# Kernel tuning notes

Hardware: AMD Instinct MI355X
Metric: run time of the kernel (lower is better)

## Reference

```python
import jax, jax.numpy as jnp
import numpy as np

LATENT = 1024

def setup_inputs() -> dict:
    key = jax.random.key(0)
    ks = jax.random.split(key, 8)
    N, BD, H, W = 1024, 2048, 7, 7
    C = 64  # num classes (pos == orient, required by stack dim=2)
    feat = jax.random.normal(ks[0], (N, BD, H, W), dtype=jnp.float32)
    fc1_w = jax.random.normal(ks[1], (LATENT, BD), dtype=jnp.float32) * (2.0 / BD) ** 0.5
    fc1_b = jnp.zeros((LATENT,), dtype=jnp.float32)
    cls_pos_w = jax.random.normal(ks[2], (C, LATENT), dtype=jnp.float32) * (2.0 / LATENT) ** 0.5
    cls_pos_b = jnp.zeros((C,), dtype=jnp.float32)
    cls_orient_w = jax.random.normal(ks[3], (C, LATENT), dtype=jnp.float32) * (2.0 / LATENT) ** 0.5
    cls_orient_b = jnp.zeros((C,), dtype=jnp.float32)
    reg_pos_w = jax.random.normal(ks[4], (C, 3, LATENT), dtype=jnp.float32) * (2.0 / LATENT) ** 0.5
    reg_pos_b = jnp.zeros((C, 3), dtype=jnp.float32)
    reg_orient_w = jax.random.normal(ks[5], (C, 4, LATENT), dtype=jnp.float32) * (2.0 / LATENT) ** 0.5
    reg_orient_b = jnp.zeros((C, 4), dtype=jnp.float32)
    return {"feat": feat, "fc1_w": fc1_w, "fc1_b": fc1_b,
            "cls_pos_w": cls_pos_w, "cls_pos_b": cls_pos_b,
            "cls_orient_w": cls_orient_w, "cls_orient_b": cls_orient_b,
            "reg_pos_w": reg_pos_w, "reg_pos_b": reg_pos_b,
            "reg_orient_w": reg_orient_w, "reg_orient_b": reg_orient_b}

def _to_label(pred):
    # relu(sum(cumprod(pred > 0.5, dim=1)) - 1) -> int64 ordinal label
    run = jnp.cumprod((pred > 0.5).astype(jnp.int32), axis=1)
    return jnp.maximum(run.sum(axis=1) - 1, 0).astype(jnp.int32)

def reference(feat, fc1_w, fc1_b, cls_pos_w, cls_pos_b, cls_orient_w, cls_orient_b,
              reg_pos_w, reg_pos_b, reg_orient_w, reg_orient_b):
    # AdaptiveAvgPool2d(1) + flatten -> [N, backbone_dim]
    x = feat.mean(axis=(2, 3))
    # fc1 + ReLU (dropout is identity at inference)
    x = jax.nn.relu(x @ fc1_w.T + fc1_b)  # [N, latent]
    cls_x = jax.nn.sigmoid(x @ cls_pos_w.T + cls_pos_b)      # [N, C]
    cls_q = jax.nn.sigmoid(x @ cls_orient_w.T + cls_orient_b)  # [N, C]
    idx_x = _to_label(cls_x)
    idx_q = _to_label(cls_q)
    # Hard-routed expert heads: gather per-sample expert weights, batched matvec
    p_x = jnp.einsum('nkd,nd->nk', reg_pos_w[idx_x], x) + reg_pos_b[idx_x]        # [N, 3]
    p_q = jnp.einsum('nkd,nd->nk', reg_orient_w[idx_q], x) + reg_orient_b[idx_q]  # [N, 4]
    pose = jnp.concatenate([p_x, p_q], axis=1)       # [N, 7]
    pose_cls = jnp.stack([cls_x, cls_q], axis=2)     # [N, C, 2]
    return pose, pose_cls
```

## Files before the change

kernel.cpp:

```cpp
#include <hip/hip_runtime.h>
#include <hip/hip_bf16.h>

#define N_SAMP   1024
#define BD       2048
#define LATENT_D 1024
#define NCLS     64
#define HW       49

typedef __attribute__((ext_vector_type(8))) _Float16 f16x8;
typedef __attribute__((ext_vector_type(4))) float f32x4;
typedef unsigned short u16;

__device__ __forceinline__ size_t split_idx_r(int row, int k, int rows) {
    const int kg = k >> 5, ke = k & 31;
    const int c2 = (ke * 2) ^ (((row >> 1) & 3) << 4);
    return ((size_t)(kg * rows + row) * 32) + (c2 >> 1);
}

__device__ __forceinline__ void split2(float v, u16* p0, u16* p1, size_t idx) {
    _Float16 h0 = (_Float16)v;
    _Float16 h1 = (_Float16)(v - (float)h0);
    p0[idx] = *(u16*)&h0;
    p1[idx] = *(u16*)&h1;
}

#define GLL16(g, l) __builtin_amdgcn_global_load_lds( \
    (const __attribute__((address_space(1))) void*)(g), \
    (__attribute__((address_space(3))) void*)(l), 16, 0, 0)

__global__ __launch_bounds__(256) void prep_kernel(const float* __restrict__ feat,
                                                   const float* __restrict__ W,
                                                   const float* __restrict__ Wp,
                                                   const float* __restrict__ Wo,
                                                   u16* __restrict__ a0,
                                                   u16* __restrict__ a1,
                                                   u16* __restrict__ b0,
                                                   u16* __restrict__ b1,
                                                   u16* __restrict__ c0,
                                                   u16* __restrict__ c1) {
    __shared__ float buf[256 * HW];
    const int b = blockIdx.x;
    const int tid = threadIdx.x;
    if (b < 8192) {
        const int lane = tid & 63, wv = tid >> 6;
        const float* src = feat + (size_t)b * (256 * HW);
        for (int c = wv; c < 49; c += 4)
            GLL16(src + c * 256 + lane * 4, (char*)buf + c * 1024 + lane * 16);
        asm volatile("s_waitcnt vmcnt(0)" ::: "memory");
        __syncthreads();
        const float* p = buf + tid * HW;
        float s = 0.f;
        #pragma unroll
        for (int k = 0; k < HW; ++k) s += p[k];
        const float v = s * (1.0f / 49.0f);
        const int n = b >> 3;
        const int d = (b & 7) * 256 + tid;
        split2(v, a0, a1, split_idx_r(n, d, N_SAMP));
    } else if (b < 16384) {
        const int b2 = b - 8192;
        const int row = b2 >> 3;
        const int d = (b2 & 7) * 256 + tid;
        split2(W[(size_t)row * BD + d], b0, b1, split_idx_r(row, d, LATENT_D));
    } else {
        const int b2 = b - 16384;
        const int row = b2 >> 2;
        const int d = (b2 & 3) * 256 + tid;
        const float v = row < 64 ? Wp[(size_t)row * LATENT_D + d]
                                 : Wo[(size_t)(row - 64) * LATENT_D + d];
        split2(v, c0, c1, split_idx_r(row, d, 128));
    }
}

__global__ __launch_bounds__(256, 2) void split_mfma(
    const u16* __restrict__ A0, const u16* __restrict__ A1,
    const u16* __restrict__ B0, const u16* __restrict__ B1,
    float* __restrict__ part, int ksteps, int rowsA, int rowsB, int ldc) {
    __shared__ u16 lds[2][4 * 4096];
    const int nwg = gridDim.x * gridDim.y * gridDim.z;
    const int flat = blockIdx.x + gridDim.x * (blockIdx.y + gridDim.y * blockIdx.z);
    const int chunk = nwg >> 3;
    const int swz = (flat & 7) * chunk + (flat >> 3);
    const int bn = swz % gridDim.x;
    const int rest = swz / gridDim.x;
    const int bm = rest % gridDim.y;
    const int kz = rest / gridDim.y;

    const int tid = threadIdx.x, lane = tid & 63, wv = tid >> 6;
    const int wrow = (wv >> 1) * 64, wcol = (wv & 1) * 64;
    const int r15 = lane & 15, khi = lane >> 4;

    const u16* gA[2] = {A0, A1};
    const u16* gB[2] = {B0, B1};
    const int kg0 = kz * ksteps;

    auto stage = [&](int kg, int buf) {
        #pragma unroll
        for (int s = 0; s < 2; ++s) {
            const u16* g = gA[s] + ((size_t)(kg * rowsA + bm * 128 + wv * 32) * 32) + lane * 8;
            u16* l = &lds[buf][s * 4096 + wv * 1024 + lane * 8];
            GLL16(g, l);
            GLL16(g + 512, l + 512);
        }
        #pragma unroll
        for (int s = 0; s < 2; ++s) {
            const u16* g = gB[s] + ((size_t)(kg * rowsB + bn * 128 + wv * 32) * 32) + lane * 8;
            u16* l = &lds[buf][(2 + s) * 4096 + wv * 1024 + lane * 8];
            GLL16(g, l);
            GLL16(g + 512, l + 512);
        }
    };

    f32x4 acc[4][4];
    #pragma unroll
    for (int i = 0; i < 4; ++i)
        #pragma unroll
        for (int j = 0; j < 4; ++j) acc[i][j] = (f32x4){0.f, 0.f, 0.f, 0.f};

    stage(kg0, 0);

    int cur = 0;
    for (int ks = 0; ks < ksteps; ++ks) {
        if (ks + 1 < ksteps) {
            stage(kg0 + ks + 1, cur ^ 1);
            asm volatile("s_waitcnt vmcnt(8)" ::: "memory");
        } else {
            asm volatile("s_waitcnt vmcnt(0)" ::: "memory");
        }
        __builtin_amdgcn_s_barrier();
        __builtin_amdgcn_sched_barrier(0);
        f16x8 af[4][2], bf[4][2];
        #pragma unroll
        for (int i = 0; i < 4; ++i) {
            const int rowA = wrow + i * 16 + r15;
            const int offA = rowA * 64 + ((khi * 16) ^ (((rowA >> 1) & 3) << 4));
            const int rowB = wcol + i * 16 + r15;
            const int offB = rowB * 64 + ((khi * 16) ^ (((rowB >> 1) & 3) << 4));
            #pragma unroll
            for (int s = 0; s < 2; ++s) {
                af[i][s] = *(const f16x8*)((const char*)&lds[cur][s * 4096] + offA);
                bf[i][s] = *(const f16x8*)((const char*)&lds[cur][(2 + s) * 4096] + offB);
            }
        }
        #pragma unroll
        for (int p = 0; p < 3; ++p) {
            const int pa = (p == 2) ? 1 : 0;
            const int pb = (p == 1) ? 1 : 0;
            #pragma unroll
            for (int i = 0; i < 4; ++i)
                #pragma unroll
                for (int j = 0; j < 4; ++j)
                    acc[i][j] = __builtin_amdgcn_mfma_f32_16x16x32_f16(
                        af[i][pa], bf[j][pb], acc[i][j], 0, 0, 0);
        }
        __builtin_amdgcn_s_barrier();
        cur ^= 1;
    }

    float* pt = part + (size_t)kz * ((size_t)N_SAMP * ldc);
    #pragma unroll
    for (int i = 0; i < 4; ++i) {
        const int row0 = bm * 128 + wrow + i * 16 + khi * 4;
        #pragma unroll
        for (int j = 0; j < 4; ++j) {
            const int col = bn * 128 + wcol + j * 16 + r15;
            #pragma unroll
            for (int q = 0; q < 4; ++q)
                pt[(size_t)(row0 + q) * ldc + col] = acc[i][j][q];
        }
    }
}

__global__ __launch_bounds__(256, 4) void cls_mfma(
    const u16* __restrict__ A0, const u16* __restrict__ A1,
    const u16* __restrict__ B0, const u16* __restrict__ B1,
    float* __restrict__ part, int ksteps) {
    __shared__ u16 lds[2][4 * 2048];
    const int nwg = gridDim.x * gridDim.y * gridDim.z;
    const int flat = blockIdx.x + gridDim.x * (blockIdx.y + gridDim.y * blockIdx.z);
    const int chunk = nwg >> 3;
    const int swz = (flat & 7) * chunk + (flat >> 3);
    const int bn = swz % gridDim.x;
    const int rest = swz / gridDim.x;
    const int bm = rest % gridDim.y;
    const int kz = rest / gridDim.y;

    const int tid = threadIdx.x, lane = tid & 63, wv = tid >> 6;
    const int wrow = (wv >> 1) * 32, wcol = (wv & 1) * 32;
    const int r15 = lane & 15, khi = lane >> 4;

    const u16* gA[2] = {A0, A1};
    const u16* gB[2] = {B0, B1};
    const int kg0 = kz * ksteps;

    auto stage = [&](int kg, int buf) {
        #pragma unroll
        for (int s = 0; s < 2; ++s) {
            const u16* g = gA[s] + ((size_t)(kg * 1024 + bm * 64 + wv * 16) * 32) + lane * 8;
            GLL16(g, &lds[buf][s * 2048 + wv * 512 + lane * 8]);
        }
        #pragma unroll
        for (int s = 0; s < 2; ++s) {
            const u16* g = gB[s] + ((size_t)(kg * 128 + bn * 64 + wv * 16) * 32) + lane * 8;
            GLL16(g, &lds[buf][(2 + s) * 2048 + wv * 512 + lane * 8]);
        }
    };

    f32x4 acc[2][2];
    #pragma unroll
    for (int i = 0; i < 2; ++i)
        #pragma unroll
        for (int j = 0; j < 2; ++j) acc[i][j] = (f32x4){0.f, 0.f, 0.f, 0.f};

    stage(kg0, 0);

    int cur = 0;
    for (int ks = 0; ks < ksteps; ++ks) {
        if (ks + 1 < ksteps) {
            stage(kg0 + ks + 1, cur ^ 1);
            asm volatile("s_waitcnt vmcnt(4)" ::: "memory");
        } else {
            asm volatile("s_waitcnt vmcnt(0)" ::: "memory");
        }
        __builtin_amdgcn_s_barrier();
        __builtin_amdgcn_sched_barrier(0);
        f16x8 af[2][2], bf[2][2];
        #pragma unroll
        for (int i = 0; i < 2; ++i) {
            const int rowA = wrow + i * 16 + r15;
            const int offA = rowA * 64 + ((khi * 16) ^ (((rowA >> 1) & 3) << 4));
            const int rowB = wcol + i * 16 + r15;
            const int offB = rowB * 64 + ((khi * 16) ^ (((rowB >> 1) & 3) << 4));
            #pragma unroll
            for (int s = 0; s < 2; ++s) {
                af[i][s] = *(const f16x8*)((const char*)&lds[cur][s * 2048] + offA);
                bf[i][s] = *(const f16x8*)((const char*)&lds[cur][(2 + s) * 2048] + offB);
            }
        }
        #pragma unroll
        for (int p = 0; p < 3; ++p) {
            const int pa = (p == 2) ? 1 : 0;
            const int pb = (p == 1) ? 1 : 0;
            #pragma unroll
            for (int i = 0; i < 2; ++i)
                #pragma unroll
                for (int j = 0; j < 2; ++j)
                    acc[i][j] = __builtin_amdgcn_mfma_f32_16x16x32_f16(
                        af[i][pa], bf[j][pb], acc[i][j], 0, 0, 0);
        }
        __builtin_amdgcn_s_barrier();
        cur ^= 1;
    }

    float* pt = part + (size_t)kz * ((size_t)N_SAMP * 128);
    #pragma unroll
    for (int i = 0; i < 2; ++i) {
        const int row0 = bm * 64 + wrow + i * 16 + khi * 4;
        #pragma unroll
        for (int j = 0; j < 2; ++j) {
            const int col = bn * 64 + wcol + j * 16 + r15;
            #pragma unroll
            for (int q = 0; q < 4; ++q)
                pt[(size_t)(row0 + q) * 128 + col] = acc[i][j][q];
        }
    }
}

__global__ __launch_bounds__(256) void reduce_fc1(const float* __restrict__ part,
                                                  const float* __restrict__ bias,
                                                  float* __restrict__ x,
                                                  u16* __restrict__ x0,
                                                  u16* __restrict__ x1,
                                                  int nsplit) {
    const int i = blockIdx.x * 256 + threadIdx.x;
    const float4* p = reinterpret_cast<const float4*>(part);
    float4 s = p[i];
    for (int z = 1; z < nsplit; ++z) {
        const float4 t = p[(size_t)z * 262144 + i];
        s.x += t.x; s.y += t.y; s.z += t.z; s.w += t.w;
    }
    const float4 b = reinterpret_cast<const float4*>(bias)[i & 255];
    s.x = fmaxf(s.x + b.x, 0.f); s.y = fmaxf(s.y + b.y, 0.f);
    s.z = fmaxf(s.z + b.z, 0.f); s.w = fmaxf(s.w + b.w, 0.f);
    reinterpret_cast<float4*>(x)[i] = s;
    const int n = i >> 8, d0 = (i & 255) * 4;
    split2(s.x, x0, x1, split_idx_r(n, d0 + 0, N_SAMP));
    split2(s.y, x0, x1, split_idx_r(n, d0 + 1, N_SAMP));
    split2(s.z, x0, x1, split_idx_r(n, d0 + 2, N_SAMP));
    split2(s.w, x0, x1, split_idx_r(n, d0 + 3, N_SAMP));
}

__global__ __launch_bounds__(128) void decode_expert(const float* __restrict__ part2,
                                                     const float* __restrict__ bp,
                                                     const float* __restrict__ bo,
                                                     const float* __restrict__ x,
                                                     const float* __restrict__ wpos,
                                                     const float* __restrict__ bpos,
                                                     const float* __restrict__ wori,
                                                     const float* __restrict__ bori,
                                                     float* __restrict__ pose_cls,
                                                     float* __restrict__ pose,
                                                     int nsplit) {
    const int n = blockIdx.x, t = threadIdx.x;
    __shared__ float xs[LATENT_D];
    __shared__ int esh[2];

    const float4* x4 = reinterpret_cast<const float4*>(x + (size_t)n * LATENT_D);
    float4* xs4 = reinterpret_cast<float4*>(xs);
    xs4[t] = x4[t];
    xs4[t + 128] = x4[t + 128];

    float s = (t < 64) ? bp[t] : bo[t - 64];
    for (int z = 0; z < nsplit; ++z)
        s += part2[(size_t)z * (N_SAMP * 128) + (size_t)n * 128 + t];
    const float sig = 1.0f / (1.0f + expf(-s));
    const int head = t >> 6, c = t & 63;
    pose_cls[(size_t)n * (NCLS * 2) + c * 2 + head] = sig;

    const unsigned long long mask = __ballot(s > 0.0f);
    if (c == 0) {
        const unsigned long long inv = ~mask;
        const int run = inv ? __builtin_ctzll(inv) : 64;
        const int lab = run - 1;
        esh[head] = lab > 0 ? lab : 0;
    }
    __syncthreads();

    const int e = esh[head];
    const int nk = head ? 4 : 3;
    for (int kk = 0; kk < nk; ++kk) {
        const float* wr = head ? wori + (size_t)(e * 4 + kk) * LATENT_D
                               : wpos + (size_t)(e * 3 + kk) * LATENT_D;
        const float bb = head ? bori[e * 4 + kk] : bpos[e * 3 + kk];
        const float4* w4 = reinterpret_cast<const float4*>(wr);
        float s2 = 0.f;
        #pragma unroll
        for (int i = 0; i < 4; ++i) {
            const int q = c + i * 64;
            const float4 a = w4[q];
            s2 += a.x * xs[q * 4] + a.y * xs[q * 4 + 1] + a.z * xs[q * 4 + 2] + a.w * xs[q * 4 + 3];
        }
        #pragma unroll
        for (int off = 32; off > 0; off >>= 1) s2 += __shfl_down(s2, off);
        if (c == 0) pose[(size_t)n * 7 + (head ? 3 + kk : kk)] = s2 + bb;
    }
}

extern "C" void kernel_launch(void* const* d_in, const int* in_sizes, int n_in,
                              void* d_out, int out_size, void* d_ws, size_t ws_size,
                              hipStream_t stream) {
    const float* feat   = (const float*)d_in[0];
    const float* fc1_w  = (const float*)d_in[1];
    const float* fc1_b  = (const float*)d_in[2];
    const float* cpw    = (const float*)d_in[3];
    const float* cpb    = (const float*)d_in[4];
    const float* cow    = (const float*)d_in[5];
    const float* cob    = (const float*)d_in[6];
    const float* rpw    = (const float*)d_in[7];
    const float* rpb    = (const float*)d_in[8];
    const float* row_   = (const float*)d_in[9];
    const float* rob    = (const float*)d_in[10];

    float* out = (float*)d_out;
    float* pose     = out;
    float* pose_cls = out + (size_t)N_SAMP * 7;

    char* ws = (char*)d_ws;
    const size_t MB = (size_t)1 << 20;
    size_t off = 0;
    auto take = [&](size_t bytes) { char* p = ws + off; off += (bytes + 255) & ~(size_t)255; return p; };

    u16* A0 = (u16*)take(4 * MB);
    u16* A1 = (u16*)take(4 * MB);
    u16* B0 = (u16*)take(4 * MB);
    u16* B1 = (u16*)take(4 * MB);
    u16* C0 = (u16*)take(256 * 1024);
    u16* C1 = (u16*)take(256 * 1024);
    u16* X0 = (u16*)take(2 * MB);
    u16* X1 = (u16*)take(2 * MB);
    float* x = (float*)take(4 * MB);

    int nsplit = 8;
    while (nsplit > 1 && off + (size_t)nsplit * 4 * MB + 5 * MB > ws_size) nsplit >>= 1;
    float* part = (float*)take((size_t)nsplit * 4 * MB);
    int nsplit_c = 8;
    while (nsplit_c > 1 && off + (size_t)nsplit_c * 512 * 1024 > ws_size) nsplit_c >>= 1;
    float* part2 = (float*)take((size_t)nsplit_c * 512 * 1024);

    prep_kernel<<<16896, 256, 0, stream>>>(feat, fc1_w, cpw, cow,
                                           A0, A1, B0, B1, C0, C1);
    split_mfma<<<dim3(8, 8, nsplit), 256, 0, stream>>>(
        A0, A1, B0, B1, part, 64 / nsplit, N_SAMP, LATENT_D, LATENT_D);
    reduce_fc1<<<1024, 256, 0, stream>>>(part, fc1_b, x, X0, X1, nsplit);
    cls_mfma<<<dim3(2, 16, nsplit_c), 256, 0, stream>>>(
        X0, X1, C0, C1, part2, 32 / nsplit_c);
    decode_expert<<<N_SAMP, 128, 0, stream>>>(part2, cpb, cob, x, rpw, rpb, row_, rob,
                                              pose_cls, pose, nsplit_c);
}
```

Before: 126.3 us.

## Fuse split-K reduction into fc1 GEMM via last-block atomic counter

```diff
diff --git a/kernel.cpp b/kernel.cpp
--- a/kernel.cpp
+++ b/kernel.cpp
@@ -37,7 +37,8 @@
                                                    u16* __restrict__ b0,
                                                    u16* __restrict__ b1,
                                                    u16* __restrict__ c0,
-                                                   u16* __restrict__ c1) {
+                                                   u16* __restrict__ c1,
+                                                   int* __restrict__ counters) {
     __shared__ float buf[256 * HW];
     const int b = blockIdx.x;
     const int tid = threadIdx.x;
@@ -61,21 +62,27 @@
         const int row = b2 >> 3;
         const int d = (b2 & 7) * 256 + tid;
         split2(W[(size_t)row * BD + d], b0, b1, split_idx_r(row, d, LATENT_D));
-    } else {
+    } else if (b < 16896) {
         const int b2 = b - 16384;
         const int row = b2 >> 2;
         const int d = (b2 & 3) * 256 + tid;
         const float v = row < 64 ? Wp[(size_t)row * LATENT_D + d]
                                  : Wo[(size_t)(row - 64) * LATENT_D + d];
         split2(v, c0, c1, split_idx_r(row, d, 128));
+    } else {
+        if (tid < 64) counters[tid] = 0;
     }
 }
 
 __global__ __launch_bounds__(256, 2) void split_mfma(
     const u16* __restrict__ A0, const u16* __restrict__ A1,
     const u16* __restrict__ B0, const u16* __restrict__ B1,
-    float* __restrict__ part, int ksteps, int rowsA, int rowsB, int ldc) {
+    float* __restrict__ part, int ksteps,
+    const float* __restrict__ bias, float* __restrict__ x,
+    u16* __restrict__ x0, u16* __restrict__ x1,
+    int* __restrict__ counters) {
     __shared__ u16 lds[2][4 * 4096];
+    __shared__ int is_last;
     const int nwg = gridDim.x * gridDim.y * gridDim.z;
     const int flat = blockIdx.x + gridDim.x * (blockIdx.y + gridDim.y * blockIdx.z);
     const int chunk = nwg >> 3;
@@ -96,14 +103,14 @@
     auto stage = [&](int kg, int buf) {
         #pragma unroll
         for (int s = 0; s < 2; ++s) {
-            const u16* g = gA[s] + ((size_t)(kg * rowsA + bm * 128 + wv * 32) * 32) + lane * 8;
+            const u16* g = gA[s] + ((size_t)(kg * N_SAMP + bm * 128 + wv * 32) * 32) + lane * 8;
             u16* l = &lds[buf][s * 4096 + wv * 1024 + lane * 8];
             GLL16(g, l);
             GLL16(g + 512, l + 512);
         }
         #pragma unroll
         for (int s = 0; s < 2; ++s) {
-            const u16* g = gB[s] + ((size_t)(kg * rowsB + bn * 128 + wv * 32) * 32) + lane * 8;
+            const u16* g = gB[s] + ((size_t)(kg * LATENT_D + bn * 128 + wv * 32) * 32) + lane * 8;
             u16* l = &lds[buf][(2 + s) * 4096 + wv * 1024 + lane * 8];
             GLL16(g, l);
             GLL16(g + 512, l + 512);
@@ -156,7 +163,7 @@
         cur ^= 1;
     }
 
-    float* pt = part + (size_t)kz * ((size_t)N_SAMP * ldc);
+    float* pt = part + ((size_t)kz << 20);
     #pragma unroll
     for (int i = 0; i < 4; ++i) {
         const int row0 = bm * 128 + wrow + i * 16 + khi * 4;
@@ -165,8 +172,41 @@
             const int col = bn * 128 + wcol + j * 16 + r15;
             #pragma unroll
             for (int q = 0; q < 4; ++q)
-                pt[(size_t)(row0 + q) * ldc + col] = acc[i][j][q];
-        }
+                pt[(size_t)(row0 + q) * LATENT_D + col] = acc[i][j][q];
+        }
+    }
+
+    __threadfence();
+    __syncthreads();
+    if (tid == 0) {
+        const int old = __hip_atomic_fetch_add(&counters[bm * 8 + bn], 1,
+                                               __ATOMIC_ACQ_REL,
+                                               __HIP_MEMORY_SCOPE_AGENT);
+        is_last = (old == (int)gridDim.z - 1);
+    }
+    __syncthreads();
+    if (!is_last) return;
+    __threadfence();
+
+    const int nsplit = gridDim.z;
+    for (int e = tid; e < 4096; e += 256) {
+        const int r = e >> 5, c4 = e & 31;
+        const int row = bm * 128 + r;
+        const int col = bn * 128 + c4 * 4;
+        const float* pp = part + (size_t)row * LATENT_D + col;
+        float4 s = *(const float4*)pp;
+        for (int z = 1; z < nsplit; ++z) {
+            const float4 t = *(const float4*)(pp + ((size_t)z << 20));
+            s.x += t.x; s.y += t.y; s.z += t.z; s.w += t.w;
+        }
+        const float4 bb = reinterpret_cast<const float4*>(bias)[bn * 32 + c4];
+        s.x = fmaxf(s.x + bb.x, 0.f); s.y = fmaxf(s.y + bb.y, 0.f);
+        s.z = fmaxf(s.z + bb.z, 0.f); s.w = fmaxf(s.w + bb.w, 0.f);
+        *reinterpret_cast<float4*>(x + (size_t)row * LATENT_D + col) = s;
+        split2(s.x, x0, x1, split_idx_r(row, col + 0, N_SAMP));
+        split2(s.y, x0, x1, split_idx_r(row, col + 1, N_SAMP));
+        split2(s.z, x0, x1, split_idx_r(row, col + 2, N_SAMP));
+        split2(s.w, x0, x1, split_idx_r(row, col + 3, N_SAMP));
     }
 }
 
@@ -263,30 +303,6 @@
                 pt[(size_t)(row0 + q) * 128 + col] = acc[i][j][q];
         }
     }
-}
-
-__global__ __launch_bounds__(256) void reduce_fc1(const float* __restrict__ part,
-                                                  const float* __restrict__ bias,
-                                                  float* __restrict__ x,
-                                                  u16* __restrict__ x0,
-                                                  u16* __restrict__ x1,
-                                                  int nsplit) {
-    const int i = blockIdx.x * 256 + threadIdx.x;
-    const float4* p = reinterpret_cast<const float4*>(part);
-    float4 s = p[i];
-    for (int z = 1; z < nsplit; ++z) {
-        const float4 t = p[(size_t)z * 262144 + i];
-        s.x += t.x; s.y += t.y; s.z += t.z; s.w += t.w;
-    }
-    const float4 b = reinterpret_cast<const float4*>(bias)[i & 255];
-    s.x = fmaxf(s.x + b.x, 0.f); s.y = fmaxf(s.y + b.y, 0.f);
-    s.z = fmaxf(s.z + b.z, 0.f); s.w = fmaxf(s.w + b.w, 0.f);
-    reinterpret_cast<float4*>(x)[i] = s;
-    const int n = i >> 8, d0 = (i & 255) * 4;
-    split2(s.x, x0, x1, split_idx_r(n, d0 + 0, N_SAMP));
-    split2(s.y, x0, x1, split_idx_r(n, d0 + 1, N_SAMP));
-    split2(s.z, x0, x1, split_idx_r(n, d0 + 2, N_SAMP));
-    split2(s.w, x0, x1, split_idx_r(n, d0 + 3, N_SAMP));
 }
 
 __global__ __launch_bounds__(128) void decode_expert(const float* __restrict__ part2,
@@ -378,19 +394,19 @@
     u16* X0 = (u16*)take(2 * MB);
     u16* X1 = (u16*)take(2 * MB);
     float* x = (float*)take(4 * MB);
-
-    int nsplit = 8;
-    while (nsplit > 1 && off + (size_t)nsplit * 4 * MB + 5 * MB > ws_size) nsplit >>= 1;
+    int* counters = (int*)take(1024);
+
+    int nsplit = 4;
+    while (nsplit > 1 && off + (size_t)nsplit * 4 * MB + 4 * MB > ws_size) nsplit >>= 1;
     float* part = (float*)take((size_t)nsplit * 4 * MB);
     int nsplit_c = 8;
     while (nsplit_c > 1 && off + (size_t)nsplit_c * 512 * 1024 > ws_size) nsplit_c >>= 1;
     float* part2 = (float*)take((size_t)nsplit_c * 512 * 1024);
 
-    prep_kernel<<<16896, 256, 0, stream>>>(feat, fc1_w, cpw, cow,
-                                           A0, A1, B0, B1, C0, C1);
+    prep_kernel<<<16897, 256, 0, stream>>>(feat, fc1_w, cpw, cow,
+                                           A0, A1, B0, B1, C0, C1, counters);
     split_mfma<<<dim3(8, 8, nsplit), 256, 0, stream>>>(
-        A0, A1, B0, B1, part, 64 / nsplit, N_SAMP, LATENT_D, LATENT_D);
-    reduce_fc1<<<1024, 256, 0, stream>>>(part, fc1_b, x, X0, X1, nsplit);
+        A0, A1, B0, B1, part, 64 / nsplit, fc1_b, x, X0, X1, counters);
     cls_mfma<<<dim3(2, 16, nsplit_c), 256, 0, stream>>>(
         X0, X1, C0, C1, part2, 32 / nsplit_c);
     decode_expert<<<N_SAMP, 128, 0, stream>>>(part2, cpb, cob, x, rpw, rpb, row_, rob,
```

Measured after the change: 198.9 us. +57.5%, slower.
